# Optimization experiments

Hardware: AMD Instinct MI355X
Metric: run time of the kernel (lower is better)

The kernel has to match this reference:

```python
import jax, jax.numpy as jnp
import numpy as np

N = 100000
E = 1600000
IN_CH, HID_CH, OUT_CH = 128, 64, 32


def setup_inputs() -> dict:
    key = jax.random.key(0)
    ks = jax.random.split(key, 6)
    x = jax.random.normal(ks[0], (N, IN_CH), dtype=jnp.float32)
    ei = jax.random.randint(ks[1], (2, E), 0, N, dtype=jnp.int64)
    W1 = jax.random.normal(ks[2], (IN_CH, HID_CH), dtype=jnp.float32) * 0.05
    b1 = jax.random.normal(ks[3], (HID_CH,), dtype=jnp.float32) * 0.05
    W2 = jax.random.normal(ks[4], (HID_CH, OUT_CH), dtype=jnp.float32) * 0.05
    b2 = jax.random.normal(ks[5], (OUT_CH,), dtype=jnp.float32) * 0.05
    return {"x": x, "ei": ei, "W1": W1, "b1": b1, "W2": W2, "b2": b2}


def gcn_layer(x, sa, da, n):
    # degree with self-loops already appended in sa/da
    deg = jax.ops.segment_sum(jnp.ones((sa.shape[0],), x.dtype), da, num_segments=n)
    prod = deg[sa] * deg[da]
    norm = jnp.where(prod > 0, jax.lax.rsqrt(prod), 0.0)  # (deg_s*deg_d)^-0.5, inf->0
    msg = x[sa] * norm[:, None]            # [E+N, C] gather + scale
    return jax.ops.segment_sum(msg, da, num_segments=n)  # scatter_add


def reference(x, ei, W1, b1, W2, b2):
    n = x.shape[0]
    loop = jnp.arange(n, dtype=ei.dtype)
    sa = jnp.concatenate([ei[0], loop])
    da = jnp.concatenate([ei[1], loop])
    h = gcn_layer(x @ W1 + b1, sa, da, n)
    h = jax.nn.relu(h)
    # dropout: eval mode (training=False) -> identity
    return gcn_layer(h @ W2 + b2, sa, da, n)
```

## Files before the change

### kernel.cpp

```cpp
#include <hip/hip_runtime.h>

#define NN 100000
#define NE 1600000
#define IN_CH 128
#define HID_CH 64
#define OUT_CH 32
#define NBUCK 391
#define CHUNKA 8192

typedef unsigned short ushort_t;
typedef _Float16 half2_t __attribute__((ext_vector_type(2)));

__device__ inline ushort_t f2bf(float f) {
    union { float f; unsigned u; } v; v.f = f;
    unsigned r = v.u + 0x7fff + ((v.u >> 16) & 1);
    return (ushort_t)(r >> 16);
}
__device__ inline float blo(unsigned u) {
    union { unsigned x; float f; } v; v.x = u << 16; return v.f;
}
__device__ inline float bhi(unsigned u) {
    union { unsigned x; float f; } v; v.x = u & 0xffff0000u; return v.f;
}
__device__ inline unsigned pkh(float a, float b) {
    union { half2_t h; unsigned u; } v;
    v.h[0] = (_Float16)a; v.h[1] = (_Float16)b;
    return v.u;
}
__device__ inline half2_t u2h(unsigned u) {
    union { unsigned u; half2_t h; } v; v.u = u; return v.h;
}
__device__ inline float fdot2(unsigned a, unsigned b, float c) {
#if __has_builtin(__builtin_amdgcn_fdot2)
    return __builtin_amdgcn_fdot2(u2h(a), u2h(b), c, false);
#else
    half2_t ha = u2h(a), hb = u2h(b);
    return c + (float)ha[0] * (float)hb[0] + (float)ha[1] * (float)hb[1];
#endif
}

__global__ __launch_bounds__(256) void k_bhist(const int* __restrict__ da,
                                               int* __restrict__ bcnt) {
    __shared__ int hist[NBUCK];
    int t = threadIdx.x;
    for (int i = t; i < NBUCK; i += 256) hist[i] = 0;
    __syncthreads();
    int base = blockIdx.x * CHUNKA;
    for (int i = 0; i < CHUNKA; i += 256) {
        int e = base + i + t;
        if (e < NE) atomicAdd(&hist[da[e] >> 8], 1);
    }
    __syncthreads();
    for (int i = t; i < NBUCK; i += 256) {
        int c = hist[i];
        if (c) atomicAdd(&bcnt[i], c);
    }
}

__global__ __launch_bounds__(512) void k_bscan(const int* __restrict__ bcnt,
                                               int* __restrict__ bbase,
                                               int* __restrict__ bcur,
                                               int* __restrict__ rowptr) {
    __shared__ int lds[512];
    int t = threadIdx.x;
    int v = (t < NBUCK) ? bcnt[t] : 0;
    lds[t] = v;
    __syncthreads();
    for (int off = 1; off < 512; off <<= 1) {
        int x = (t >= off) ? lds[t - off] : 0;
        __syncthreads();
        lds[t] += x;
        __syncthreads();
    }
    int excl = lds[t] - v;
    if (t < NBUCK) { bbase[t] = excl; bcur[t] = excl; }
    if (t == 0) { bbase[NBUCK] = NE; rowptr[NN] = NE; }
}

__global__ __launch_bounds__(256) void k_bfill(const int* __restrict__ sa,
                                               const int* __restrict__ da,
                                               int* __restrict__ bcur,
                                               unsigned* __restrict__ ebuf) {
    __shared__ int hist[NBUCK];
    __shared__ int lcur[NBUCK];
    int t = threadIdx.x;
    for (int i = t; i < NBUCK; i += 256) hist[i] = 0;
    __syncthreads();
    int base = blockIdx.x * CHUNKA;
    for (int i = 0; i < CHUNKA; i += 256) {
        int e = base + i + t;
        if (e < NE) atomicAdd(&hist[da[e] >> 8], 1);
    }
    __syncthreads();
    for (int b = t; b < NBUCK; b += 256) {
        int c = hist[b];
        lcur[b] = c ? atomicAdd(&bcur[b], c) : 0;
    }
    __syncthreads();
    for (int i = 0; i < CHUNKA; i += 256) {
        int e = base + i + t;
        if (e < NE) {
            int d = da[e];
            int p = atomicAdd(&lcur[d >> 8], 1);
            ebuf[p] = ((unsigned)sa[e] << 8) | (unsigned)(d & 255);
        }
    }
}

__global__ __launch_bounds__(256) void k_bfine(const unsigned* __restrict__ ebuf,
                                               const int* __restrict__ bbase,
                                               int* __restrict__ rowptr,
                                               float* __restrict__ rs,
                                               int* __restrict__ col) {
    __shared__ int cnt[256];
    __shared__ int cur[256];
    __shared__ int scn[256];
    int b = blockIdx.x, t = threadIdx.x;
    int nb = NN - b * 256; if (nb > 256) nb = 256;
    int beg = bbase[b], end = bbase[b + 1];
    cnt[t] = 0;
    __syncthreads();
    for (int i = beg + t; i < end; i += 256) atomicAdd(&cnt[ebuf[i] & 255], 1);
    __syncthreads();
    int v = cnt[t];
    scn[t] = v;
    __syncthreads();
    for (int off = 1; off < 256; off <<= 1) {
        int x = (t >= off) ? scn[t - off] : 0;
        __syncthreads();
        scn[t] += x;
        __syncthreads();
    }
    int excl = scn[t] - v;
    if (t < nb) {
        rowptr[b * 256 + t] = beg + excl;
        rs[b * 256 + t] = rsqrtf((float)(v + 1));
        cur[t] = beg + excl;
    }
    __syncthreads();
    for (int i = beg + t; i < end; i += 256) {
        unsigned p = ebuf[i];
        int pos = atomicAdd(&cur[p & 255], 1);
        col[pos] = (int)(p >> 8);
    }
}

#define SWZU1(n, k2) ((n) * 64 + ((k2) ^ ((((n) & 7)) << 2)))
#define SWZ2(n, k) ((n) * 64 + ((k) ^ ((((n) & 7)) << 2)))

__global__ __launch_bounds__(256, 4) void k_gemm1(
    const float* __restrict__ x, const float* __restrict__ W1,
    const float* __restrict__ b1, const float* __restrict__ rs,
    ushort_t* __restrict__ xsb) {
    __shared__ unsigned xth[64 * 64];
    __shared__ unsigned w1h[64 * 64];
    int t = threadIdx.x;
    int base = blockIdx.x * 64;

#pragma unroll
    for (int i = 0; i < 8; ++i) {
        int flat = i * 1024 + t * 4;
        int node = flat >> 7, k0 = flat & 127;
        int gn = base + node;
        float4 v = make_float4(0.f, 0.f, 0.f, 0.f);
        if (gn < NN) v = *(const float4*)(x + (size_t)gn * IN_CH + k0);
        uint2 pk;
        pk.x = pkh(v.x, v.y);
        pk.y = pkh(v.z, v.w);
        *(uint2*)&xth[SWZU1(node, k0 >> 1)] = pk;
    }
#pragma unroll
    for (int i = 0; i < 16; ++i) {
        int idx = i * 256 + t;
        int k2 = idx >> 6, c = idx & 63;
        float f0 = W1[(2 * k2) * 64 + c];
        float f1 = W1[(2 * k2 + 1) * 64 + c];
        w1h[idx] = pkh(f0, f1);
    }
    __syncthreads();

    int tn = t & 15, tc = t >> 4;
    int c0 = tc * 4;
    float acc[4][4];
#pragma unroll
    for (int a = 0; a < 4; ++a)
#pragma unroll
        for (int b = 0; b < 4; ++b) acc[a][b] = 0.f;

    for (int k2 = 0; k2 < 64; k2 += 2) {
        uint2 xu[4];
#pragma unroll
        for (int jn = 0; jn < 4; ++jn)
            xu[jn] = *(uint2*)&xth[SWZU1(tn + jn * 16, k2)];
        uint4 w0 = *(uint4*)&w1h[(k2 + 0) * 64 + c0];
        uint4 w1 = *(uint4*)&w1h[(k2 + 1) * 64 + c0];
        unsigned wq0[4] = {w0.x, w0.y, w0.z, w0.w};
        unsigned wq1[4] = {w1.x, w1.y, w1.z, w1.w};
#pragma unroll
        for (int jn = 0; jn < 4; ++jn)
#pragma unroll
            for (int jc = 0; jc < 4; ++jc) {
                acc[jn][jc] = fdot2(xu[jn].x, wq0[jc], acc[jn][jc]);
                acc[jn][jc] = fdot2(xu[jn].y, wq1[jc], acc[jn][jc]);
            }
    }

    float4 bb = *(const float4*)&b1[c0];
#pragma unroll
    for (int jn = 0; jn < 4; ++jn) {
        int gn = base + tn + jn * 16;
        if (gn < NN) {
            float r = rs[gn];
            uint2 pk;
            pk.x = (unsigned)f2bf((acc[jn][0] + bb.x) * r) |
                   ((unsigned)f2bf((acc[jn][1] + bb.y) * r) << 16);
            pk.y = (unsigned)f2bf((acc[jn][2] + bb.z) * r) |
                   ((unsigned)f2bf((acc[jn][3] + bb.w) * r) << 16);
            *(uint2*)&xsb[(size_t)gn * HID_CH + c0] = pk;
        }
    }
}

__global__ __launch_bounds__(256) void k_agg1(
    const int* __restrict__ rowptr, const int* __restrict__ col,
    const ushort_t* __restrict__ xsb, const float* __restrict__ rs,
    ushort_t* __restrict__ hb) {
    int gid = blockIdx.x * blockDim.x + threadIdx.x;
    int n = gid >> 6;
    if (n >= NN) return;
    int lane = threadIdx.x & 63;
    int g = lane >> 4;
    unsigned c0 = (unsigned)(lane & 15) * 4;
    int beg = rowptr[n], end = rowptr[n + 1];

    float a0 = 0.f, a1 = 0.f, a2 = 0.f, a3 = 0.f;
    if (g == 0) {
        uint2 sv = *(const uint2*)&xsb[(unsigned)n * 64u + c0];
        a0 = blo(sv.x); a1 = bhi(sv.x); a2 = blo(sv.y); a3 = bhi(sv.y);
    }

    int i = beg;
    for (; i + 16 <= end; i += 16) {
        int s0 = col[i + g];
        int s1 = col[i + 4 + g];
        int s2 = col[i + 8 + g];
        int s3 = col[i + 12 + g];
        uint2 v0 = *(const uint2*)&xsb[(unsigned)s0 * 64u + c0];
        uint2 v1 = *(const uint2*)&xsb[(unsigned)s1 * 64u + c0];
        uint2 v2 = *(const uint2*)&xsb[(unsigned)s2 * 64u + c0];
        uint2 v3 = *(const uint2*)&xsb[(unsigned)s3 * 64u + c0];
        a0 += blo(v0.x); a1 += bhi(v0.x); a2 += blo(v0.y); a3 += bhi(v0.y);
        a0 += blo(v1.x); a1 += bhi(v1.x); a2 += blo(v1.y); a3 += bhi(v1.y);
        a0 += blo(v2.x); a1 += bhi(v2.x); a2 += blo(v2.y); a3 += bhi(v2.y);
        a0 += blo(v3.x); a1 += bhi(v3.x); a2 += blo(v3.y); a3 += bhi(v3.y);
    }
    for (; i + 4 <= end; i += 4) {
        int s0 = col[i + g];
        uint2 v0 = *(const uint2*)&xsb[(unsigned)s0 * 64u + c0];
        a0 += blo(v0.x); a1 += bhi(v0.x); a2 += blo(v0.y); a3 += bhi(v0.y);
    }
    int r = end - i;
    if (g < r) {
        int s0 = col[i + g];
        uint2 v0 = *(const uint2*)&xsb[(unsigned)s0 * 64u + c0];
        a0 += blo(v0.x); a1 += bhi(v0.x); a2 += blo(v0.y); a3 += bhi(v0.y);
    }

    a0 += __shfl_xor(a0, 16); a1 += __shfl_xor(a1, 16);
    a2 += __shfl_xor(a2, 16); a3 += __shfl_xor(a3, 16);
    a0 += __shfl_xor(a0, 32); a1 += __shfl_xor(a1, 32);
    a2 += __shfl_xor(a2, 32); a3 += __shfl_xor(a3, 32);

    if (g == 0) {
        float rn = rs[n];
        uint2 pk;
        pk.x = (unsigned)f2bf(fmaxf(a0 * rn, 0.f)) |
               ((unsigned)f2bf(fmaxf(a1 * rn, 0.f)) << 16);
        pk.y = (unsigned)f2bf(fmaxf(a2 * rn, 0.f)) |
               ((unsigned)f2bf(fmaxf(a3 * rn, 0.f)) << 16);
        *(uint2*)&hb[(unsigned)n * 64u + c0] = pk;
    }
}

__global__ __launch_bounds__(256) void k_gemm2(
    const ushort_t* __restrict__ hb, const float* __restrict__ W2,
    const float* __restrict__ b2, const float* __restrict__ rs,
    ushort_t* __restrict__ ysb) {
    __shared__ float ht[64 * 64];
    __shared__ float w2s[64 * 32];
    int t = threadIdx.x;
    int base = blockIdx.x * 64;

#pragma unroll
    for (int i = 0; i < 8; ++i) {
        int uidx = i * 256 + t;
        int node = uidx >> 5, k2 = uidx & 31;
        int gn = base + node;
        unsigned u = 0;
        if (gn < NN) u = *(const unsigned*)&hb[(size_t)gn * HID_CH + k2 * 2];
        float2 f; f.x = blo(u); f.y = bhi(u);
        *(float2*)&ht[SWZ2(node, k2 * 2)] = f;
    }
#pragma unroll
    for (int i = 0; i < 2; ++i) {
        int flat = i * 1024 + t * 4;
        *(float4*)&w2s[flat] = *(const float4*)(W2 + flat);
    }
    __syncthreads();

    int tn = t & 15, tc = t >> 4;
    int c0 = tc * 2;
    float acc[4][2];
#pragma unroll
    for (int a = 0; a < 4; ++a) { acc[a][0] = 0.f; acc[a][1] = 0.f; }

    for (int k0 = 0; k0 < 64; k0 += 4) {
        float xq[4][4], wq[4][2];
#pragma unroll
        for (int j = 0; j < 4; ++j)
            *(float2*)&wq[j][0] = *(float2*)&w2s[(k0 + j) * 32 + c0];
#pragma unroll
        for (int jn = 0; jn < 4; ++jn)
            *(float4*)&xq[jn][0] = *(float4*)&ht[SWZ2(tn + jn * 16, k0)];
#pragma unroll
        for (int jn = 0; jn < 4; ++jn)
#pragma unroll
            for (int j = 0; j < 4; ++j) {
                acc[jn][0] = fmaf(xq[jn][j], wq[j][0], acc[jn][0]);
                acc[jn][1] = fmaf(xq[jn][j], wq[j][1], acc[jn][1]);
            }
    }

    float2 bb = *(const float2*)&b2[c0];
#pragma unroll
    for (int jn = 0; jn < 4; ++jn) {
        int gn = base + tn + jn * 16;
        if (gn < NN) {
            float r = rs[gn];
            unsigned pk = (unsigned)f2bf((acc[jn][0] + bb.x) * r) |
                          ((unsigned)f2bf((acc[jn][1] + bb.y) * r) << 16);
            *(unsigned*)&ysb[(size_t)gn * OUT_CH + c0] = pk;
        }
    }
}

__global__ __launch_bounds__(256) void k_agg2(
    const int* __restrict__ rowptr, const int* __restrict__ col,
    const ushort_t* __restrict__ ysb, const float* __restrict__ rs,
    float* __restrict__ out) {
    int gid = blockIdx.x * blockDim.x + threadIdx.x;
    int n = gid >> 6;
    if (n >= NN) return;
    int lane = threadIdx.x & 63;
    int g = lane >> 3;
    unsigned c0 = (unsigned)(lane & 7) * 4;
    int beg = rowptr[n], end = rowptr[n + 1];

    float a0 = 0.f, a1 = 0.f, a2 = 0.f, a3 = 0.f;
    if (g == 0) {
        uint2 sv = *(const uint2*)&ysb[(unsigned)n * 32u + c0];
        a0 = blo(sv.x); a1 = bhi(sv.x); a2 = blo(sv.y); a3 = bhi(sv.y);
    }

    int i = beg;
    for (; i + 16 <= end; i += 16) {
        int s0 = col[i + g];
        int s1 = col[i + 8 + g];
        uint2 v0 = *(const uint2*)&ysb[(unsigned)s0 * 32u + c0];
        uint2 v1 = *(const uint2*)&ysb[(unsigned)s1 * 32u + c0];
        a0 += blo(v0.x); a1 += bhi(v0.x); a2 += blo(v0.y); a3 += bhi(v0.y);
        a0 += blo(v1.x); a1 += bhi(v1.x); a2 += blo(v1.y); a3 += bhi(v1.y);
    }
    if (i + 8 <= end) {
        int s0 = col[i + g];
        uint2 v0 = *(const uint2*)&ysb[(unsigned)s0 * 32u + c0];
        a0 += blo(v0.x); a1 += bhi(v0.x); a2 += blo(v0.y); a3 += bhi(v0.y);
        i += 8;
    }
    int r = end - i;
    if (g < r) {
        int s0 = col[i + g];
        uint2 v0 = *(const uint2*)&ysb[(unsigned)s0 * 32u + c0];
        a0 += blo(v0.x); a1 += bhi(v0.x); a2 += blo(v0.y); a3 += bhi(v0.y);
    }

    a0 += __shfl_xor(a0, 8);  a1 += __shfl_xor(a1, 8);
    a2 += __shfl_xor(a2, 8);  a3 += __shfl_xor(a3, 8);
    a0 += __shfl_xor(a0, 16); a1 += __shfl_xor(a1, 16);
    a2 += __shfl_xor(a2, 16); a3 += __shfl_xor(a3, 16);
    a0 += __shfl_xor(a0, 32); a1 += __shfl_xor(a1, 32);
    a2 += __shfl_xor(a2, 32); a3 += __shfl_xor(a3, 32);

    if (g == 0) {
        float rn = rs[n];
        float4 o;
        o.x = a0 * rn; o.y = a1 * rn; o.z = a2 * rn; o.w = a3 * rn;
        *(float4*)&out[(size_t)n * OUT_CH + c0] = o;
    }
}

extern "C" void kernel_launch(void* const* d_in, const int* in_sizes, int n_in,
                              void* d_out, int out_size, void* d_ws, size_t ws_size,
                              hipStream_t stream) {
    const float* x  = (const float*)d_in[0];
    const int*   ei = (const int*)d_in[1];
    const float* W1 = (const float*)d_in[2];
    const float* b1 = (const float*)d_in[3];
    const float* W2 = (const float*)d_in[4];
    const float* b2 = (const float*)d_in[5];
    const int* sa = ei;
    const int* da = ei + NE;

    char* ws = (char*)d_ws;
    size_t off = 0;
    auto alloc = [&](size_t bytes) {
        void* p = ws + off;
        off += (bytes + 255) & ~(size_t)255;
        return p;
    };
    int*      bcnt   = (int*)alloc((size_t)NBUCK * 4);
    int*      bbase  = (int*)alloc((size_t)(NBUCK + 1) * 4);
    int*      bcur   = (int*)alloc((size_t)NBUCK * 4);
    int*      rowptr = (int*)alloc((size_t)(NN + 1) * 4);
    float*    rs     = (float*)alloc((size_t)NN * 4);
    unsigned* ebuf   = (unsigned*)alloc((size_t)NE * 4);
    int*      col    = (int*)alloc((size_t)NE * 4);
    ushort_t* xsb    = (ushort_t*)alloc((size_t)NN * HID_CH * 2);
    ushort_t* hb     = (ushort_t*)alloc((size_t)NN * HID_CH * 2);
    ushort_t* ysb    = (ushort_t*)alloc((size_t)NN * OUT_CH * 2);
    float*    outp   = (float*)d_out;

    const int B = 256;
    const int NBLKA = (NE + CHUNKA - 1) / CHUNKA;
    hipMemsetAsync(bcnt, 0, (size_t)NBUCK * 4, stream);
    k_bhist<<<NBLKA, 256, 0, stream>>>(da, bcnt);
    k_bscan<<<1, 512, 0, stream>>>(bcnt, bbase, bcur, rowptr);
    k_bfill<<<NBLKA, 256, 0, stream>>>(sa, da, bcur, ebuf);
    k_bfine<<<NBUCK, 256, 0, stream>>>(ebuf, bbase, rowptr, rs, col);

    const int NBLK_GEMM = (NN + 63) / 64;
    k_gemm1<<<NBLK_GEMM, 256, 0, stream>>>(x, W1, b1, rs, xsb);
    k_agg1<<<(NN * 64 + B - 1) / B, B, 0, stream>>>(rowptr, col, xsb, rs, hb);
    k_gemm2<<<NBLK_GEMM, 256, 0, stream>>>(hb, W2, b2, rs, ysb);
    k_agg2<<<(NN * 64 + B - 1) / B, B, 0, stream>>>(rowptr, col, ysb, rs, outp);
}
```

Baseline: 222.4 us.

## Privatize per-wave LDS histograms, halve bucket chunk size, split agg1 launch

```diff
diff --git a/kernel.cpp b/kernel.cpp
--- a/kernel.cpp
+++ b/kernel.cpp
@@ -6,7 +6,8 @@
 #define HID_CH 64
 #define OUT_CH 32
 #define NBUCK 391
-#define CHUNKA 8192
+#define CHUNKH 4096
+#define CHUNKF 4096
 
 typedef unsigned short ushort_t;
 typedef _Float16 half2_t __attribute__((ext_vector_type(2)));
@@ -41,18 +42,18 @@
 
 __global__ __launch_bounds__(256) void k_bhist(const int* __restrict__ da,
                                                int* __restrict__ bcnt) {
-    __shared__ int hist[NBUCK];
-    int t = threadIdx.x;
-    for (int i = t; i < NBUCK; i += 256) hist[i] = 0;
-    __syncthreads();
-    int base = blockIdx.x * CHUNKA;
-    for (int i = 0; i < CHUNKA; i += 256) {
+    __shared__ int hist[4][NBUCK];
+    int t = threadIdx.x, w = t >> 6;
+    for (int i = t; i < 4 * NBUCK; i += 256) ((int*)hist)[i] = 0;
+    __syncthreads();
+    int base = blockIdx.x * CHUNKH;
+    for (int i = 0; i < CHUNKH; i += 256) {
         int e = base + i + t;
-        if (e < NE) atomicAdd(&hist[da[e] >> 8], 1);
+        if (e < NE) atomicAdd(&hist[w][da[e] >> 8], 1);
     }
     __syncthreads();
     for (int i = t; i < NBUCK; i += 256) {
-        int c = hist[i];
+        int c = hist[0][i] + hist[1][i] + hist[2][i] + hist[3][i];
         if (c) atomicAdd(&bcnt[i], c);
     }
 }
@@ -81,27 +82,27 @@
                                                const int* __restrict__ da,
                                                int* __restrict__ bcur,
                                                unsigned* __restrict__ ebuf) {
-    __shared__ int hist[NBUCK];
-    __shared__ int lcur[NBUCK];
-    int t = threadIdx.x;
-    for (int i = t; i < NBUCK; i += 256) hist[i] = 0;
-    __syncthreads();
-    int base = blockIdx.x * CHUNKA;
-    for (int i = 0; i < CHUNKA; i += 256) {
+    __shared__ int hist[4][NBUCK];
+    __shared__ int lcur[4][NBUCK];
+    int t = threadIdx.x, w = t >> 6, lane = t & 63;
+    for (int i = t; i < 4 * NBUCK; i += 256) ((int*)hist)[i] = 0;
+    __syncthreads();
+    int base = blockIdx.x * CHUNKF;
+    for (int i = 0; i < CHUNKF; i += 256) {
         int e = base + i + t;
-        if (e < NE) atomicAdd(&hist[da[e] >> 8], 1);
-    }
-    __syncthreads();
-    for (int b = t; b < NBUCK; b += 256) {
-        int c = hist[b];
-        lcur[b] = c ? atomicAdd(&bcur[b], c) : 0;
-    }
-    __syncthreads();
-    for (int i = 0; i < CHUNKA; i += 256) {
+        if (e < NE) atomicAdd(&hist[w][da[e] >> 8], 1);
+    }
+    __syncthreads();
+    for (int b = lane; b < NBUCK; b += 64) {
+        int c = hist[w][b];
+        lcur[w][b] = c ? atomicAdd(&bcur[b], c) : 0;
+    }
+    __syncthreads();
+    for (int i = 0; i < CHUNKF; i += 256) {
         int e = base + i + t;
         if (e < NE) {
             int d = da[e];
-            int p = atomicAdd(&lcur[d >> 8], 1);
+            int p = atomicAdd(&lcur[w][d >> 8], 1);
             ebuf[p] = ((unsigned)sa[e] << 8) | (unsigned)(d & 255);
         }
     }
@@ -224,10 +225,10 @@
 __global__ __launch_bounds__(256) void k_agg1(
     const int* __restrict__ rowptr, const int* __restrict__ col,
     const ushort_t* __restrict__ xsb, const float* __restrict__ rs,
-    ushort_t* __restrict__ hb) {
+    ushort_t* __restrict__ hb, int n0, int n1) {
     int gid = blockIdx.x * blockDim.x + threadIdx.x;
-    int n = gid >> 6;
-    if (n >= NN) return;
+    int n = n0 + (gid >> 6);
+    if (n >= n1) return;
     int lane = threadIdx.x & 63;
     int g = lane >> 4;
     unsigned c0 = (unsigned)(lane & 15) * 4;
@@ -431,16 +432,19 @@
     float*    outp   = (float*)d_out;
 
     const int B = 256;
-    const int NBLKA = (NE + CHUNKA - 1) / CHUNKA;
+    const int NBLKH = (NE + CHUNKH - 1) / CHUNKH;
+    const int NBLKF = (NE + CHUNKF - 1) / CHUNKF;
     hipMemsetAsync(bcnt, 0, (size_t)NBUCK * 4, stream);
-    k_bhist<<<NBLKA, 256, 0, stream>>>(da, bcnt);
+    k_bhist<<<NBLKH, 256, 0, stream>>>(da, bcnt);
     k_bscan<<<1, 512, 0, stream>>>(bcnt, bbase, bcur, rowptr);
-    k_bfill<<<NBLKA, 256, 0, stream>>>(sa, da, bcur, ebuf);
+    k_bfill<<<NBLKF, 256, 0, stream>>>(sa, da, bcur, ebuf);
     k_bfine<<<NBUCK, 256, 0, stream>>>(ebuf, bbase, rowptr, rs, col);
 
     const int NBLK_GEMM = (NN + 63) / 64;
     k_gemm1<<<NBLK_GEMM, 256, 0, stream>>>(x, W1, b1, rs, xsb);
-    k_agg1<<<(NN * 64 + B - 1) / B, B, 0, stream>>>(rowptr, col, xsb, rs, hb);
+    const int HALF = NN / 2;
+    k_agg1<<<(HALF * 64 + B - 1) / B, B, 0, stream>>>(rowptr, col, xsb, rs, hb, 0, HALF);
+    k_agg1<<<((NN - HALF) * 64 + B - 1) / B, B, 0, stream>>>(rowptr, col, xsb, rs, hb, HALF, NN);
     k_gemm2<<<NBLK_GEMM, 256, 0, stream>>>(hb, W2, b2, rs, ysb);
     k_agg2<<<(NN * 64 + B - 1) / B, B, 0, stream>>>(rowptr, col, ysb, rs, outp);
 }
```

New measurement: 266.0 us. 19.6% more time.
